# Kernel optimization log

Hardware: AMD Instinct MI355X
Metric: run time of the kernel (lower is better)

## Reference

```python
import jax, jax.numpy as jnp
import numpy as np
import math

B, S, D, H = 1, 2048, 4096, 32
HD = D // H
FF = 11008
EPS = 1e-5
THETA = 10000.0


def rms_norm(x, w, eps=EPS):
    # use_mean=False, elementwise_scale=True, high-precision pow -> RMSNorm in fp32
    xf = x.astype(jnp.float32)
    inv = jax.lax.rsqrt(jnp.mean(xf * xf, axis=-1, keepdims=True) + eps)
    return ((xf * inv).astype(x.dtype)) * w


def rope(x, theta=THETA):
    # x: [b, s, h, hd]; interleaved (adjacent-pair) rotary as in LLaMA/FMS
    s, hd = x.shape[1], x.shape[-1]
    inv_freq = 1.0 / (theta ** (jnp.arange(0, hd, 2, dtype=jnp.float32) / hd))
    ang = jnp.arange(s, dtype=jnp.float32)[:, None] * inv_freq[None, :]  # [s, hd/2]
    cos = jnp.cos(ang)[None, :, None, :].astype(x.dtype)
    sin = jnp.sin(ang)[None, :, None, :].astype(x.dtype)
    x1 = x[..., 0::2]
    x2 = x[..., 1::2]
    r1 = x1 * cos - x2 * sin
    r2 = x1 * sin + x2 * cos
    return jnp.stack([r1, r2], axis=-1).reshape(x.shape)


def block_forward(x, ln_w, ff_ln_w, wq, wk, wv, wo, wg, w1, w2):
    residual = x
    xn = rms_norm(x, ln_w)
    b, s, d = xn.shape
    q = rope((xn @ wq).reshape(b, s, H, HD))
    k = rope((xn @ wk).reshape(b, s, H, HD))
    v = (xn @ wv).reshape(b, s, H, HD)
    scores = jnp.einsum('bqhd,bkhd->bhqk', q, k) / math.sqrt(HD)
    causal = jnp.tril(jnp.ones((s, s), dtype=bool))
    scores = jnp.where(causal[None, None], scores, jnp.finfo(scores.dtype).min)
    probs = jax.nn.softmax(scores, axis=-1)
    attn = jnp.einsum('bhqk,bkhd->bqhd', probs, v).reshape(b, s, d)
    x = attn @ wo + residual

    residual = x
    xn = rms_norm(x, ff_ln_w)
    h = jax.nn.silu(xn @ wg) * (xn @ w1)  # swish-gated GLU
    x = h @ w2 + residual
    return x


def setup_inputs() -> dict:
    key = jax.random.key(0)
    ks = jax.random.split(key, 8)
    sc = lambda fan_in: 1.0 / math.sqrt(fan_in)
    return {
        'x': jax.random.normal(ks[0], (B, S, D), jnp.float32),
        'ln_w': jnp.ones((D,), jnp.float32),
        'ff_ln_w': jnp.ones((D,), jnp.float32),
        'wq': jax.random.normal(ks[1], (D, D), jnp.float32) * sc(D),
        'wk': jax.random.normal(ks[2], (D, D), jnp.float32) * sc(D),
        'wv': jax.random.normal(ks[3], (D, D), jnp.float32) * sc(D),
        'wo': jax.random.normal(ks[4], (D, D), jnp.float32) * sc(D),
        'wg': jax.random.normal(ks[5], (D, FF), jnp.float32) * sc(D),
        'w1': jax.random.normal(ks[6], (D, FF), jnp.float32) * sc(D),
        'w2': jax.random.normal(ks[7], (FF, D), jnp.float32) * sc(FF),
    }


def reference(x, ln_w, ff_ln_w, wq, wk, wv, wo, wg, w1, w2):
    return block_forward(x, ln_w, ff_ln_w, wq, wk, wv, wo, wg, w1, w2)
```

## Files before the change

kernel.cpp:

```cpp
#include <hip/hip_runtime.h>
#include <cstdint>
#include <cmath>


typedef unsigned short u16;
typedef unsigned int u32;
typedef __bf16 bf16x8 __attribute__((ext_vector_type(8)));
typedef float f32x4 __attribute__((ext_vector_type(4)));

__device__ __forceinline__ float bf2f(u16 u) {
    u32 x = ((u32)u) << 16; float f; __builtin_memcpy(&f, &x, 4); return f;
}
__device__ __forceinline__ u16 f2bf(float f) {
    u32 x; __builtin_memcpy(&x, &f, 4);
    u32 r = x + 0x7fff + ((x >> 16) & 1);
    return (u16)(r >> 16);
}

__device__ __forceinline__ void g2l16(const void* g, void* l) {
    auto* gp = reinterpret_cast<const u32*>(reinterpret_cast<uintptr_t>(g));
    auto* lp = reinterpret_cast<__attribute__((address_space(3))) u32*>(
        reinterpret_cast<uintptr_t>(l));
    __builtin_amdgcn_global_load_lds(gp, lp, 16, 0, 0);
}

__global__ __launch_bounds__(256) void transpose_f32_bf16(
    const float* __restrict__ in, u16* __restrict__ out, int K, int N) {
    __shared__ float tile[64][33];
    const int k0 = blockIdx.y * 64, n0 = blockIdx.x * 32;
    const int x = threadIdx.x, y = threadIdx.y;
#pragma unroll
    for (int i = 0; i < 8; i++) {
        int kr = y + i * 8;
        tile[kr][x] = in[(size_t)(k0 + kr) * N + n0 + x];
    }
    __syncthreads();
#pragma unroll
    for (int i = 0; i < 4; i++) {
        int nr = y + i * 8;
        u32 pk = (u32)f2bf(tile[2 * x][nr]) | ((u32)f2bf(tile[2 * x + 1][nr]) << 16);
        ((u32*)(out + (size_t)(n0 + nr) * K + k0))[x] = pk;
    }
}

__global__ __launch_bounds__(256) void rmsnorm_kernel(
    const float* __restrict__ x, const float* __restrict__ w, u16* __restrict__ o) {
    const int row = blockIdx.x;
    const float4* xr = (const float4*)(x + (size_t)row * 4096);
    float4 v[4];
    float ss = 0.f;
#pragma unroll
    for (int i = 0; i < 4; i++) {
        v[i] = xr[threadIdx.x + 256 * i];
        ss += v[i].x * v[i].x + v[i].y * v[i].y + v[i].z * v[i].z + v[i].w * v[i].w;
    }
#pragma unroll
    for (int off = 32; off > 0; off >>= 1) ss += __shfl_down(ss, off, 64);
    __shared__ float ws4[4];
    if ((threadIdx.x & 63) == 0) ws4[threadIdx.x >> 6] = ss;
    __syncthreads();
    float inv = rsqrtf((ws4[0] + ws4[1] + ws4[2] + ws4[3]) * (1.f / 4096.f) + 1e-5f);
    const float4* wr = (const float4*)w;
    u32* orow = (u32*)(o + (size_t)row * 4096);
#pragma unroll
    for (int i = 0; i < 4; i++) {
        float4 wv = wr[threadIdx.x + 256 * i];
        u32 lo = (u32)f2bf(v[i].x * inv * wv.x) | ((u32)f2bf(v[i].y * inv * wv.y) << 16);
        u32 hi = (u32)f2bf(v[i].z * inv * wv.z) | ((u32)f2bf(v[i].w * inv * wv.w) << 16);
        int idx = (threadIdx.x + 256 * i) * 2;
        orow[idx] = lo; orow[idx + 1] = hi;
    }
}

__global__ __launch_bounds__(256) void rope_kernel(u16* __restrict__ q, u16* __restrict__ k) {
    const int s = blockIdx.x;
    u32* pr = (u32*)((blockIdx.y ? k : q) + (size_t)s * 4096);
#pragma unroll
    for (int it = 0; it < 8; it++) {
        int pidx = threadIdx.x + it * 256;
        int i = pidx & 63;
        float ang = (float)s * expf(-(float)i * 0.14391156832817f);
        float sn, cs; sincosf(ang, &sn, &cs);
        u32 u = pr[pidx];
        float x1 = bf2f((u16)u), x2 = bf2f((u16)(u >> 16));
        pr[pidx] = (u32)f2bf(x1 * cs - x2 * sn) | ((u32)f2bf(x1 * sn + x2 * cs) << 16);
    }
}

__global__ __launch_bounds__(256) void silu_mul_kernel(
    const u16* __restrict__ g, const u16* __restrict__ u, u16* __restrict__ o) {
    size_t i = (size_t)blockIdx.x * 256 + threadIdx.x;
    uint4 gv = ((const uint4*)g)[i];
    uint4 uv = ((const uint4*)u)[i];
    const u32* gp = (const u32*)&gv;
    const u32* up = (const u32*)&uv;
    u32 rr[4];
#pragma unroll
    for (int j = 0; j < 4; j++) {
        float g0 = bf2f((u16)gp[j]), g1 = bf2f((u16)(gp[j] >> 16));
        float u0 = bf2f((u16)up[j]), u1 = bf2f((u16)(up[j] >> 16));
        float s0 = g0 / (1.f + __expf(-g0)) * u0;
        float s1 = g1 / (1.f + __expf(-g1)) * u1;
        rr[j] = (u32)f2bf(s0) | ((u32)f2bf(s1) << 16);
    }
    ((uint4*)o)[i] = *(const uint4*)rr;
}

template <int EPI>
__global__ __launch_bounds__(256) void gemm_bt(
    const u16* __restrict__ A, const u16* __restrict__ BT, void* __restrict__ Cout,
    const float* __restrict__ res, int M, int N, int K, int lda, int ldb, int ldc) {
    (void)M; (void)N;
    __shared__ u16 As[128 * 32];
    __shared__ u16 Bs[128 * 32];
    const int tid = threadIdx.x;
    const int lane = tid & 63, wave = tid >> 6;
    const int m0 = blockIdx.y * 128, n0 = blockIdx.x * 128;
    const int wm = (wave >> 1) * 64, wn = (wave & 1) * 64;
    const int gc = lane & 15, grp = lane >> 4;

    const u16* ga0 = A + (size_t)(m0 + (tid >> 2)) * lda + (tid & 3) * 8;
    const u16* ga1 = ga0 + (size_t)64 * lda;
    const u16* gb0 = BT + (size_t)(n0 + (tid >> 2)) * ldb + (tid & 3) * 8;
    const u16* gb1 = gb0 + (size_t)64 * ldb;
    u16* la0 = As + tid * 8;
    u16* la1 = As + tid * 8 + 2048;
    u16* lb0 = Bs + tid * 8;
    u16* lb1 = Bs + tid * 8 + 2048;

    f32x4 acc[4][4] = {};

    for (int k0 = 0; k0 < K; k0 += 32) {
        g2l16(ga0, la0); g2l16(ga1, la1);
        g2l16(gb0, lb0); g2l16(gb1, lb1);
        ga0 += 32; ga1 += 32; gb0 += 32; gb1 += 32;
        __syncthreads();
        bf16x8 af[4], bfr[4];
#pragma unroll
        for (int t = 0; t < 4; t++) {
            af[t]  = *(const bf16x8*)(As + (wm + t * 16 + gc) * 32 + grp * 8);
            bfr[t] = *(const bf16x8*)(Bs + (wn + t * 16 + gc) * 32 + grp * 8);
        }
#pragma unroll
        for (int mt = 0; mt < 4; mt++)
#pragma unroll
            for (int nt = 0; nt < 4; nt++)
                acc[mt][nt] = __builtin_amdgcn_mfma_f32_16x16x32_bf16(
                    af[mt], bfr[nt], acc[mt][nt], 0, 0, 0);
        __syncthreads();
    }

#pragma unroll
    for (int mt = 0; mt < 4; mt++) {
#pragma unroll
        for (int nt = 0; nt < 4; nt++) {
            int row0 = m0 + wm + mt * 16 + grp * 4;
            int col = n0 + wn + nt * 16 + gc;
            if (EPI == 0) {
                u16* C = (u16*)Cout;
#pragma unroll
                for (int r = 0; r < 4; r++)
                    C[(size_t)(row0 + r) * ldc + col] = f2bf(acc[mt][nt][r]);
            } else if (EPI == 1) {
                u16* C = (u16*)Cout;
                u32 p0 = (u32)f2bf(acc[mt][nt][0]) | ((u32)f2bf(acc[mt][nt][1]) << 16);
                u32 p1 = (u32)f2bf(acc[mt][nt][2]) | ((u32)f2bf(acc[mt][nt][3]) << 16);
                u32* dst = (u32*)(C + (size_t)col * ldc + row0);
                dst[0] = p0; dst[1] = p1;
            } else {
                float* C = (float*)Cout;
#pragma unroll
                for (int r = 0; r < 4; r++) {
                    size_t idx = (size_t)(row0 + r) * ldc + col;
                    C[idx] = acc[mt][nt][r] + res[idx];
                }
            }
        }
    }
}

__global__ __launch_bounds__(512) void attn_kernel(
    const u16* __restrict__ q, const u16* __restrict__ k,
    const u16* __restrict__ vt, u16* __restrict__ o) {
    __shared__ u16 Ks[2][64][136];
    __shared__ u16 Vs[2][128][72];
    __shared__ u16 Ps[128][72];
    const int h = blockIdx.y;
    const int tid = threadIdx.x, lane = tid & 63, wave = tid >> 6;
    const int gc = lane & 15, grp = lane >> 4;
    const float scale = 0.08838834764831843f;

    const int ti0 = blockIdx.x;
    const int ti1 = 15 - (int)blockIdx.x;
    const int n0 = 2 * ti0 + 2;
    const int total = n0 + 2 * ti1 + 2;

    {
        uint4 kr0[2], vr0[2];
#pragma unroll
        for (int i = 0; i < 2; i++) {
            int c = tid + i * 512;
            kr0[i] = *(const uint4*)(k + (size_t)(c >> 4) * 4096 + h * 128 + (c & 15) * 8);
            vr0[i] = *(const uint4*)(vt + (size_t)(h * 128 + (c >> 3)) * 2048 + (c & 7) * 8);
        }
#pragma unroll
        for (int i = 0; i < 2; i++) {
            int c = tid + i * 512;
            *(uint4*)(&Ks[0][c >> 4][(c & 15) * 8]) = kr0[i];
            *(uint4*)(&Vs[0][c >> 3][(c & 7) * 8]) = vr0[i];
        }
    }
    __syncthreads();

    bf16x8 qf[4];
    f32x4 oacc[8];
    float mrun[4], lrun[4];
    const f32x4 fzero = {};
    int cur = 0;

    for (int it = 0; it < total; ++it) {
        const int t = (it >= n0) ? 1 : 0;
        const int local = t ? it - n0 : it;
        const int ti = t ? ti1 : ti0;
        const int j0 = local * 64;
        const int mw = ti * 128 + wave * 16;

        if (local == 0) {
#pragma unroll
            for (int ks = 0; ks < 4; ks++)
                qf[ks] = *(const bf16x8*)(q + (size_t)(mw + gc) * 4096 + h * 128 +
                                          ks * 32 + grp * 8);
#pragma unroll
            for (int nd = 0; nd < 8; nd++) oacc[nd] = fzero;
#pragma unroll
            for (int r = 0; r < 4; r++) { mrun[r] = -1e30f; lrun[r] = 0.f; }
        }

        const int itn = it + 1;
        const bool havenext = itn < total;
        const int jn = (itn >= n0 ? itn - n0 : itn) * 64;
        uint4 kreg[2], vreg[2];
        if (havenext) {
#pragma unroll
            for (int i = 0; i < 2; i++) {
                int c = tid + i * 512;
                kreg[i] = *(const uint4*)(k + (size_t)(jn + (c >> 4)) * 4096 +
                                          h * 128 + (c & 15) * 8);
                vreg[i] = *(const uint4*)(vt + (size_t)(h * 128 + (c >> 3)) * 2048 +
                                          jn + (c & 7) * 8);
            }
        }

        f32x4 sfr[4] = {};
#pragma unroll
        for (int ks = 0; ks < 4; ks++) {
            bf16x8 kf[4];
#pragma unroll
            for (int nt = 0; nt < 4; nt++)
                kf[nt] = *(const bf16x8*)(&Ks[cur][nt * 16 + gc][ks * 32 + grp * 8]);
#pragma unroll
            for (int nt = 0; nt < 4; nt++)
                sfr[nt] = __builtin_amdgcn_mfma_f32_16x16x32_bf16(
                    qf[ks], kf[nt], sfr[nt], 0, 0, 0);
        }

        if (j0 + 63 > mw) {
#pragma unroll
            for (int nt = 0; nt < 4; nt++)
#pragma unroll
                for (int r = 0; r < 4; r++) {
                    int rowg = mw + grp * 4 + r;
                    int colg = j0 + nt * 16 + gc;
                    if (colg > rowg) sfr[nt][r] = -3.0e38f;
                }
        }

#pragma unroll
        for (int r = 0; r < 4; r++) {
            float rm = fmaxf(fmaxf(sfr[0][r], sfr[1][r]),
                             fmaxf(sfr[2][r], sfr[3][r])) * scale;
#pragma unroll
            for (int msk = 1; msk < 16; msk <<= 1)
                rm = fmaxf(rm, __shfl_xor(rm, msk, 64));
            float mnew = fmaxf(mrun[r], rm);
            float alpha = __expf(mrun[r] - mnew);
            mrun[r] = mnew;
            float rs = 0.f;
#pragma unroll
            for (int nt = 0; nt < 4; nt++) {
                float pv = __expf(sfr[nt][r] * scale - mnew);
                sfr[nt][r] = pv;
                rs += pv;
            }
#pragma unroll
            for (int msk = 1; msk < 16; msk <<= 1) rs += __shfl_xor(rs, msk, 64);
            lrun[r] = lrun[r] * alpha + rs;
#pragma unroll
            for (int nd = 0; nd < 8; nd++) oacc[nd][r] *= alpha;
        }

#pragma unroll
        for (int nt = 0; nt < 4; nt++)
#pragma unroll
            for (int r = 0; r < 4; r++)
                Ps[wave * 16 + grp * 4 + r][nt * 16 + gc] = f2bf(sfr[nt][r]);

#pragma unroll
        for (int ks2 = 0; ks2 < 2; ks2++) {
            bf16x8 pf = *(const bf16x8*)(&Ps[wave * 16 + gc][ks2 * 32 + grp * 8]);
#pragma unroll
            for (int nd = 0; nd < 8; nd++) {
                bf16x8 vf = *(const bf16x8*)(&Vs[cur][nd * 16 + gc][ks2 * 32 + grp * 8]);
                oacc[nd] = __builtin_amdgcn_mfma_f32_16x16x32_bf16(
                    pf, vf, oacc[nd], 0, 0, 0);
            }
        }

        if (havenext) {
#pragma unroll
            for (int i = 0; i < 2; i++) {
                int c = tid + i * 512;
                *(uint4*)(&Ks[cur ^ 1][c >> 4][(c & 15) * 8]) = kreg[i];
                *(uint4*)(&Vs[cur ^ 1][c >> 3][(c & 7) * 8]) = vreg[i];
            }
        }
        __syncthreads();
        cur ^= 1;

        if (local == 2 * ti + 1) {
#pragma unroll
            for (int r = 0; r < 4; r++) {
                float invl = 1.f / lrun[r];
                int rowg = mw + grp * 4 + r;
#pragma unroll
                for (int nd = 0; nd < 8; nd++)
                    o[(size_t)rowg * 4096 + h * 128 + nd * 16 + gc] =
                        f2bf(oacc[nd][r] * invl);
            }
        }
    }
}

extern "C" void kernel_launch(void* const* d_in, const int* in_sizes, int n_in,
                              void* d_out, int out_size, void* d_ws, size_t ws_size,
                              hipStream_t stream) {
    (void)in_sizes; (void)n_in; (void)out_size; (void)ws_size;
    const float* x    = (const float*)d_in[0];
    const float* ln_w = (const float*)d_in[1];
    const float* ffw  = (const float*)d_in[2];
    const float* wq   = (const float*)d_in[3];
    const float* wk   = (const float*)d_in[4];
    const float* wv   = (const float*)d_in[5];
    const float* wo   = (const float*)d_in[6];
    const float* wg   = (const float*)d_in[7];
    const float* w1   = (const float*)d_in[8];
    const float* w2   = (const float*)d_in[9];
    float* out = (float*)d_out;

    char* p = (char*)d_ws;
    auto alloc = [&](size_t n) { char* r = p; p += (n + 255) & ~(size_t)255; return r; };
    u16* wqT = (u16*)alloc((size_t)4096 * 4096 * 2);
    u16* wkT = (u16*)alloc((size_t)4096 * 4096 * 2);
    u16* wvT = (u16*)alloc((size_t)4096 * 4096 * 2);
    u16* woT = (u16*)alloc((size_t)4096 * 4096 * 2);
    u16* wgT = (u16*)alloc((size_t)11008 * 4096 * 2);
    u16* w1T = (u16*)alloc((size_t)11008 * 4096 * 2);
    u16* w2T = (u16*)alloc((size_t)4096 * 11008 * 2);
    u16* xn  = (u16*)alloc((size_t)2048 * 4096 * 2);
    u16* qb  = (u16*)alloc((size_t)2048 * 4096 * 2);
    u16* kb  = (u16*)alloc((size_t)2048 * 4096 * 2);
    u16* vtb = (u16*)alloc((size_t)4096 * 2048 * 2);
    u16* ab  = (u16*)alloc((size_t)2048 * 4096 * 2);
    float* x2 = (float*)alloc((size_t)2048 * 4096 * 4);
    u16* xn2 = (u16*)alloc((size_t)2048 * 4096 * 2);
    u16* gb  = (u16*)alloc((size_t)2048 * 11008 * 2);
    u16* ub  = (u16*)alloc((size_t)2048 * 11008 * 2);

    dim3 tb(32, 8);
    transpose_f32_bf16<<<dim3(128, 64), tb, 0, stream>>>(wq, wqT, 4096, 4096);
    transpose_f32_bf16<<<dim3(128, 64), tb, 0, stream>>>(wk, wkT, 4096, 4096);
    transpose_f32_bf16<<<dim3(128, 64), tb, 0, stream>>>(wv, wvT, 4096, 4096);
    transpose_f32_bf16<<<dim3(128, 64), tb, 0, stream>>>(wo, woT, 4096, 4096);
    transpose_f32_bf16<<<dim3(344, 64), tb, 0, stream>>>(wg, wgT, 4096, 11008);
    transpose_f32_bf16<<<dim3(344, 64), tb, 0, stream>>>(w1, w1T, 4096, 11008);
    transpose_f32_bf16<<<dim3(128, 172), tb, 0, stream>>>(w2, w2T, 11008, 4096);

    rmsnorm_kernel<<<2048, 256, 0, stream>>>(x, ln_w, xn);

    gemm_bt<0><<<dim3(32, 16), 256, 0, stream>>>(xn, wqT, qb, nullptr,
                                                 2048, 4096, 4096, 4096, 4096, 4096);
    gemm_bt<0><<<dim3(32, 16), 256, 0, stream>>>(xn, wkT, kb, nullptr,
                                                 2048, 4096, 4096, 4096, 4096, 4096);
    gemm_bt<1><<<dim3(32, 16), 256, 0, stream>>>(xn, wvT, vtb, nullptr,
                                                 2048, 4096, 4096, 4096, 4096, 2048);

    rope_kernel<<<dim3(2048, 2), 256, 0, stream>>>(qb, kb);

    attn_kernel<<<dim3(8, 32), 512, 0, stream>>>(qb, kb, vtb, ab);

    gemm_bt<2><<<dim3(32, 16), 256, 0, stream>>>(ab, woT, x2, x,
                                                 2048, 4096, 4096, 4096, 4096, 4096);

    rmsnorm_kernel<<<2048, 256, 0, stream>>>(x2, ffw, xn2);

    gemm_bt<0><<<dim3(86, 16), 256, 0, stream>>>(xn2, wgT, gb, nullptr,
                                                 2048, 11008, 4096, 4096, 4096, 11008);
    gemm_bt<0><<<dim3(86, 16), 256, 0, stream>>>(xn2, w1T, ub, nullptr,
                                                 2048, 11008, 4096, 4096, 4096, 11008);

    silu_mul_kernel<<<11008, 256, 0, stream>>>(gb, ub, gb);

    gemm_bt<2><<<dim3(32, 16), 256, 0, stream>>>(gb, w2T, out, x2,
                                                 2048, 4096, 11008, 11008, 11008, 4096);
}
```

Before: 2.231 ms.

## Add 256x256 pipelined LDS GEMM and fuse gate/up projections into one GEMM

Introduces a new gemm8 kernel with 256x256 tiles and 512 threads. It uses direct global-to-LDS loads into a swizzled double-buffered layout, manual waitcnt and barrier scheduling, MFMA priority boosting and block-index swizzling for L2 locality. The FFN gate and up weights are concatenated so a single wide GEMM produces both. The down projection also moves to the new kernel, and silu_mul reads the interleaved gate/up buffer. The aim is better MFMA utilisation and fewer launches on the largest GEMMs. In exchange the hand-written pipeline is fragile, and the down GEMM launches only 128 blocks, which may underfill the GPU.

```diff
diff --git a/kernel.cpp b/kernel.cpp
--- a/kernel.cpp
+++ b/kernel.cpp
@@ -23,6 +23,12 @@
         reinterpret_cast<uintptr_t>(l));
     __builtin_amdgcn_global_load_lds(gp, lp, 16, 0, 0);
 }
+
+#define FENCE asm volatile("" ::: "memory")
+#define SBAR  do { FENCE; __builtin_amdgcn_s_barrier(); FENCE; } while (0)
+#define WLGKM asm volatile("s_waitcnt lgkmcnt(0)" ::: "memory")
+#define WVM6  asm volatile("s_waitcnt vmcnt(6)" ::: "memory")
+#define WVM0  asm volatile("s_waitcnt vmcnt(0)" ::: "memory")
 
 __global__ __launch_bounds__(256) void transpose_f32_bf16(
     const float* __restrict__ in, u16* __restrict__ out, int K, int N) {
@@ -88,10 +94,13 @@
 }
 
 __global__ __launch_bounds__(256) void silu_mul_kernel(
-    const u16* __restrict__ g, const u16* __restrict__ u, u16* __restrict__ o) {
-    size_t i = (size_t)blockIdx.x * 256 + threadIdx.x;
-    uint4 gv = ((const uint4*)g)[i];
-    uint4 uv = ((const uint4*)u)[i];
+    const u16* __restrict__ gu, u16* __restrict__ o) {
+    u32 i = blockIdx.x * 256 + threadIdx.x;
+    u32 row = i / 1376;
+    u32 c = i - row * 1376;
+    const uint4* grow = (const uint4*)gu + (size_t)row * 2752;
+    uint4 gv = grow[c];
+    uint4 uv = grow[c + 1376];
     const u32* gp = (const u32*)&gv;
     const u32* up = (const u32*)&uv;
     u32 rr[4];
@@ -179,6 +188,150 @@
     }
 }
 
+__device__ __forceinline__ bf16x8 frd(const u16* lds, int slotu16, int lrow, int grp) {
+    int idx = slotu16 + lrow * 32 + ((grp ^ ((lrow >> 1) & 3)) << 3);
+    return *(const bf16x8*)(lds + idx);
+}
+
+template <int EPI>
+__global__ __launch_bounds__(512, 2) void gemm8(
+    const u16* __restrict__ A, const u16* __restrict__ BT, void* __restrict__ Cout,
+    const float* __restrict__ res, int NT, int cpx, int K, int lda, int ldb, int ldc) {
+    extern __shared__ u16 lds[];
+    const int nkt = K >> 6;
+    const int bid = blockIdx.x;
+    const int swz = (bid & 7) * cpx + (bid >> 3);
+    const int mt = swz / NT, nt = swz - mt * NT;
+    const int m0 = mt << 8, n0 = nt << 8;
+    const int tid = threadIdx.x, lane = tid & 63, wave = tid >> 6;
+    const int wmi = wave >> 2, wni = wave & 3;
+    const int gc = lane & 15, grp = lane >> 4;
+
+    const int o0 = tid * 16, o1 = o0 + 8192;
+    const int p0 = o0 ^ (((o0 >> 7) & 3) << 4);
+    const int p1 = o1 ^ (((o1 >> 7) & 3) << 4);
+    const int r0 = p0 >> 6, c0 = (p0 & 63) >> 1;
+    const int r1 = p1 >> 6, c1 = (p1 & 63) >> 1;
+    const u16* gA0 = A + (size_t)(m0 + r0) * lda + c0;
+    const u16* gA1 = A + (size_t)(m0 + r1) * lda + c1;
+    const u16* gB0 = BT + (size_t)(n0 + r0) * ldb + c0;
+    const u16* gB1 = BT + (size_t)(n0 + r1) * ldb + c1;
+    u16* ld0 = lds + tid * 8;
+
+    auto STA = [&](int buf, int kh, int ktS) {
+        int slot = (buf * 2 + kh) * 8192;
+        int ko = ktS * 64 + kh * 32;
+        g2l16(gA0 + ko, ld0 + slot);
+        g2l16(gA1 + ko, ld0 + slot + 4096);
+    };
+    auto STB = [&](int buf, int kh, int ktS) {
+        int slot = 32768 + (buf * 2 + kh) * 8192;
+        int ko = ktS * 64 + kh * 32;
+        g2l16(gB0 + ko, ld0 + slot);
+        g2l16(gB1 + ko, ld0 + slot + 4096);
+    };
+
+    f32x4 acc[8][4] = {};
+    bf16x8 aA[8], aB[8], b[4];
+    const int arow = wmi * 128 + gc;
+    const int brow = wni * 64 + gc;
+
+    auto RDA = [&](bf16x8* dst, int buf, int kh) {
+        int slot = (buf * 2 + kh) * 8192;
+#pragma unroll
+        for (int m = 0; m < 8; m++) dst[m] = frd(lds, slot, arow + m * 16, grp);
+    };
+    auto RDB = [&](int buf, int kh) {
+        int slot = 32768 + (buf * 2 + kh) * 8192;
+#pragma unroll
+        for (int n = 0; n < 4; n++) b[n] = frd(lds, slot, brow + n * 16, grp);
+    };
+    auto MM = [&](const bf16x8* af, int mlo) {
+        __builtin_amdgcn_s_setprio(1);
+#pragma unroll
+        for (int m = 0; m < 4; m++)
+#pragma unroll
+            for (int n = 0; n < 4; n++)
+                acc[mlo + m][n] = __builtin_amdgcn_mfma_f32_16x16x32_bf16(
+                    af[mlo + m], b[n], acc[mlo + m][n], 0, 0, 0);
+        __builtin_amdgcn_s_setprio(0);
+    };
+
+    STA(0, 0, 0); STB(0, 0, 0); STA(0, 1, 0); STB(0, 1, 0);
+    STA(1, 0, 1); STB(1, 0, 1); STA(1, 1, 1);
+    WVM6;
+    SBAR;
+
+    for (int kt = 0; kt < nkt; kt += 2) {
+        const bool pre = (kt + 2) < nkt;
+        RDA(aA, 0, 0);
+        STB(1, 1, kt + 1);
+        SBAR; WLGKM;
+        if (kt) MM(aB, 4);
+        SBAR;
+        RDB(0, 0);
+        if (pre) STA(0, 0, kt + 2);
+        SBAR; WLGKM;
+        MM(aA, 0);
+        SBAR;
+        RDA(aB, 0, 1);
+        if (pre) STB(0, 0, kt + 2);
+        SBAR; WLGKM;
+        MM(aA, 4);
+        SBAR;
+        RDB(0, 1);
+        if (pre) STA(0, 1, kt + 2);
+        SBAR; WLGKM;
+        MM(aB, 0);
+        if (pre) { WVM6; } else { WVM0; }
+        SBAR;
+        RDA(aA, 1, 0);
+        if (pre) STB(0, 1, kt + 2);
+        SBAR; WLGKM;
+        MM(aB, 4);
+        SBAR;
+        RDB(1, 0);
+        if (pre) STA(1, 0, kt + 3);
+        SBAR; WLGKM;
+        MM(aA, 0);
+        SBAR;
+        RDA(aB, 1, 1);
+        if (pre) STB(1, 0, kt + 3);
+        SBAR; WLGKM;
+        MM(aA, 4);
+        SBAR;
+        RDB(1, 1);
+        if (pre) STA(1, 1, kt + 3);
+        SBAR; WLGKM;
+        MM(aB, 0);
+        if (pre) { WVM6; } else { WVM0; }
+        SBAR;
+    }
+    MM(aB, 4);
+
+#pragma unroll
+    for (int m = 0; m < 8; m++) {
+#pragma unroll
+        for (int n = 0; n < 4; n++) {
+            int row0 = m0 + wmi * 128 + m * 16 + grp * 4;
+            int col = n0 + wni * 64 + n * 16 + gc;
+            if (EPI == 0) {
+                u16* C = (u16*)Cout;
+#pragma unroll
+                for (int r = 0; r < 4; r++)
+                    C[(size_t)(row0 + r) * ldc + col] = f2bf(acc[m][n][r]);
+            } else {
+                float* C = (float*)Cout;
+#pragma unroll
+                for (int r = 0; r < 4; r++) {
+                    size_t idx = (size_t)(row0 + r) * ldc + col;
+                    C[idx] = acc[m][n][r] + res[idx];
+                }
+            }
+        }
+    }
+}
+
 __global__ __launch_bounds__(512) void attn_kernel(
     const u16* __restrict__ q, const u16* __restrict__ k,
     const u16* __restrict__ vt, u16* __restrict__ o) {
@@ -256,22 +409,22 @@
         for (int ks = 0; ks < 4; ks++) {
             bf16x8 kf[4];
 #pragma unroll
-            for (int nt = 0; nt < 4; nt++)
-                kf[nt] = *(const bf16x8*)(&Ks[cur][nt * 16 + gc][ks * 32 + grp * 8]);
-#pragma unroll
-            for (int nt = 0; nt < 4; nt++)
-                sfr[nt] = __builtin_amdgcn_mfma_f32_16x16x32_bf16(
-                    qf[ks], kf[nt], sfr[nt], 0, 0, 0);
+            for (int nt2 = 0; nt2 < 4; nt2++)
+                kf[nt2] = *(const bf16x8*)(&Ks[cur][nt2 * 16 + gc][ks * 32 + grp * 8]);
+#pragma unroll
+            for (int nt2 = 0; nt2 < 4; nt2++)
+                sfr[nt2] = __builtin_amdgcn_mfma_f32_16x16x32_bf16(
+                    qf[ks], kf[nt2], sfr[nt2], 0, 0, 0);
         }
 
         if (j0 + 63 > mw) {
 #pragma unroll
-            for (int nt = 0; nt < 4; nt++)
+            for (int nt2 = 0; nt2 < 4; nt2++)
 #pragma unroll
                 for (int r = 0; r < 4; r++) {
                     int rowg = mw + grp * 4 + r;
-                    int colg = j0 + nt * 16 + gc;
-                    if (colg > rowg) sfr[nt][r] = -3.0e38f;
+                    int colg = j0 + nt2 * 16 + gc;
+                    if (colg > rowg) sfr[nt2][r] = -3.0e38f;
                 }
         }
 
@@ -287,9 +440,9 @@
             mrun[r] = mnew;
             float rs = 0.f;
 #pragma unroll
-            for (int nt = 0; nt < 4; nt++) {
-                float pv = __expf(sfr[nt][r] * scale - mnew);
-                sfr[nt][r] = pv;
+            for (int nt2 = 0; nt2 < 4; nt2++) {
+                float pv = __expf(sfr[nt2][r] * scale - mnew);
+                sfr[nt2][r] = pv;
                 rs += pv;
             }
 #pragma unroll
@@ -300,10 +453,10 @@
         }
 
 #pragma unroll
-        for (int nt = 0; nt < 4; nt++)
+        for (int nt2 = 0; nt2 < 4; nt2++)
 #pragma unroll
             for (int r = 0; r < 4; r++)
-                Ps[wave * 16 + grp * 4 + r][nt * 16 + gc] = f2bf(sfr[nt][r]);
+                Ps[wave * 16 + grp * 4 + r][nt2 * 16 + gc] = f2bf(sfr[nt2][r]);
 
 #pragma unroll
         for (int ks2 = 0; ks2 < 2; ks2++) {
@@ -357,32 +510,37 @@
     const float* w2   = (const float*)d_in[9];
     float* out = (float*)d_out;
 
+    hipFuncSetAttribute(reinterpret_cast<const void*>(gemm8<0>),
+                        hipFuncAttributeMaxDynamicSharedMemorySize, 131072);
+    hipFuncSetAttribute(reinterpret_cast<const void*>(gemm8<2>),
+                        hipFuncAttributeMaxDynamicSharedMemorySize, 131072);
+
     char* p = (char*)d_ws;
     auto alloc = [&](size_t n) { char* r = p; p += (n + 255) & ~(size_t)255; return r; };
-    u16* wqT = (u16*)alloc((size_t)4096 * 4096 * 2);
-    u16* wkT = (u16*)alloc((size_t)4096 * 4096 * 2);
-    u16* wvT = (u16*)alloc((size_t)4096 * 4096 * 2);
-    u16* woT = (u16*)alloc((size_t)4096 * 4096 * 2);
-    u16* wgT = (u16*)alloc((size_t)11008 * 4096 * 2);
-    u16* w1T = (u16*)alloc((size_t)11008 * 4096 * 2);
-    u16* w2T = (u16*)alloc((size_t)4096 * 11008 * 2);
-    u16* xn  = (u16*)alloc((size_t)2048 * 4096 * 2);
-    u16* qb  = (u16*)alloc((size_t)2048 * 4096 * 2);
-    u16* kb  = (u16*)alloc((size_t)2048 * 4096 * 2);
-    u16* vtb = (u16*)alloc((size_t)4096 * 2048 * 2);
-    u16* ab  = (u16*)alloc((size_t)2048 * 4096 * 2);
+    u16* wqT  = (u16*)alloc((size_t)4096 * 4096 * 2);
+    u16* wkT  = (u16*)alloc((size_t)4096 * 4096 * 2);
+    u16* wvT  = (u16*)alloc((size_t)4096 * 4096 * 2);
+    u16* woT  = (u16*)alloc((size_t)4096 * 4096 * 2);
+    u16* wguT = (u16*)alloc((size_t)22016 * 4096 * 2);
+    u16* w2T  = (u16*)alloc((size_t)4096 * 11008 * 2);
+    u16* xn   = (u16*)alloc((size_t)2048 * 4096 * 2);
+    u16* qb   = (u16*)alloc((size_t)2048 * 4096 * 2);
+    u16* kb   = (u16*)alloc((size_t)2048 * 4096 * 2);
+    u16* vtb  = (u16*)alloc((size_t)4096 * 2048 * 2);
+    u16* ab   = (u16*)alloc((size_t)2048 * 4096 * 2);
     float* x2 = (float*)alloc((size_t)2048 * 4096 * 4);
-    u16* xn2 = (u16*)alloc((size_t)2048 * 4096 * 2);
-    u16* gb  = (u16*)alloc((size_t)2048 * 11008 * 2);
-    u16* ub  = (u16*)alloc((size_t)2048 * 11008 * 2);
+    u16* xn2  = (u16*)alloc((size_t)2048 * 4096 * 2);
+    u16* gub  = (u16*)alloc((size_t)2048 * 22016 * 2);
+    u16* gb   = (u16*)alloc((size_t)2048 * 11008 * 2);
 
     dim3 tb(32, 8);
     transpose_f32_bf16<<<dim3(128, 64), tb, 0, stream>>>(wq, wqT, 4096, 4096);
     transpose_f32_bf16<<<dim3(128, 64), tb, 0, stream>>>(wk, wkT, 4096, 4096);
     transpose_f32_bf16<<<dim3(128, 64), tb, 0, stream>>>(wv, wvT, 4096, 4096);
     transpose_f32_bf16<<<dim3(128, 64), tb, 0, stream>>>(wo, woT, 4096, 4096);
-    transpose_f32_bf16<<<dim3(344, 64), tb, 0, stream>>>(wg, wgT, 4096, 11008);
-    transpose_f32_bf16<<<dim3(344, 64), tb, 0, stream>>>(w1, w1T, 4096, 11008);
+    transpose_f32_bf16<<<dim3(344, 64), tb, 0, stream>>>(wg, wguT, 4096, 11008);
+    transpose_f32_bf16<<<dim3(344, 64), tb, 0, stream>>>(
+        w1, wguT + (size_t)11008 * 4096, 4096, 11008);
     transpose_f32_bf16<<<dim3(128, 172), tb, 0, stream>>>(w2, w2T, 11008, 4096);
 
     rmsnorm_kernel<<<2048, 256, 0, stream>>>(x, ln_w, xn);
@@ -403,13 +561,11 @@
 
     rmsnorm_kernel<<<2048, 256, 0, stream>>>(x2, ffw, xn2);
 
-    gemm_bt<0><<<dim3(86, 16), 256, 0, stream>>>(xn2, wgT, gb, nullptr,
-                                                 2048, 11008, 4096, 4096, 4096, 11008);
-    gemm_bt<0><<<dim3(86, 16), 256, 0, stream>>>(xn2, w1T, ub, nullptr,
-                                                 2048, 11008, 4096, 4096, 4096, 11008);
-
-    silu_mul_kernel<<<11008, 256, 0, stream>>>(gb, ub, gb);
-
-    gemm_bt<2><<<dim3(32, 16), 256, 0, stream>>>(gb, w2T, out, x2,
-                                                 2048, 4096, 11008, 11008, 11008, 4096);
-}
+    gemm8<0><<<688, 512, 131072, stream>>>(xn2, wguT, gub, nullptr,
+                                           86, 86, 4096, 4096, 4096, 22016);
+
+    silu_mul_kernel<<<11008, 256, 0, stream>>>(gub, gb);
+
+    gemm8<2><<<128, 512, 131072, stream>>>(gb, w2T, out, x2,
+                                           16, 16, 11008, 11008, 11008, 4096);
+}
```

After: 3.500 ms. +56.9%, slower.
